# Optimization experiments

Measured on AMD Instinct MI355X. Metric: run time of the kernel, lower is better.

## Reference

```python
import jax, jax.numpy as jnp
import numpy as np
import math

B, M, DM = 4, 4096, 1024
H, HD = 16, 64            # head_dim = hidden_dim // num_heads
SEG, DIL = 128, 2         # segment_size, dilation_rate
BLOCK_M = 64              # kernel query-block size (min(64, M))
SCALE = HD ** -0.5


def _hilbert_map(seq_len):
    # Faithful port of create_hilbert_mapping_fixed (boustrophedon scan).
    if seq_len <= 64:
        return np.arange(seq_len, dtype=np.int32)
    g = int(math.ceil(math.sqrt(seq_len)))
    mp = np.zeros(seq_len, dtype=np.int64)
    idx = 0
    for row in range(g):
        cols = range(g) if row % 2 == 0 else range(g - 1, -1, -1)
        for col in cols:
            if idx < seq_len:
                lp = row * g + col
                if lp < seq_len:
                    mp[lp] = idx
                    idx += 1
    for i in range(seq_len):
        if i >= idx:
            mp[i] = i
    return mp.astype(np.int32)


def setup_inputs() -> dict:
    key = jax.random.key(0)
    k1, k2, k3 = jax.random.split(key, 3)
    x = jax.random.normal(k1, (B, M, DM), jnp.float32)
    Wqkv = jax.random.normal(k2, (3 * DM, DM), jnp.float32) * 0.02
    Wout = jax.random.normal(k3, (DM, DM), jnp.float32) * 0.02
    hmap = jnp.asarray(_hilbert_map(M))
    return {"x": x, "Wqkv": Wqkv, "Wout": Wout, "hmap": hmap}


def _hilbert_attention(x, Wqkv, Wout, hmap):
    Bn, Mn, _ = x.shape
    qkv = x @ Wqkv.T                                   # [B,M,3*DM]
    qkv = qkv.reshape(Bn, Mn, 3, H, HD).transpose(2, 0, 3, 1, 4)
    q, k, v = qkv[0], qkv[1], qkv[2]                   # [B,H,M,HD]

    S = Mn // SEG           # number of segments
    T = SEG // DIL          # keys per segment (dilated offsets 0, DIL, 2*DIL, ...)
    NB = SEG // BLOCK_M     # query blocks per segment

    # Queries gathered through Hilbert map, pre-scaled (as in kernel).
    qh = q[:, :, hmap, :] * SCALE                      # [B,H,M,HD]

    # Dilated key positions per segment, gathered through Hilbert map.
    key_pos = (jnp.arange(S)[:, None] * SEG + jnp.arange(T)[None, :] * DIL).reshape(-1)
    kh = k[:, :, hmap[key_pos], :].reshape(Bn, H, S, T, HD)
    vh = v[:, :, hmap[key_pos], :].reshape(Bn, H, S, T, HD)

    # Scores per (query-block within segment, key): [B,H,S,NB,BLOCK_M,T]
    qs = qh.reshape(Bn, H, S, NB, BLOCK_M, HD)
    scores = jnp.einsum('bhsnqd,bhstd->bhsnqt', qs, kh)

    # Kernel quirk (faithful): per-KEY max taken over the 64-query block,
    # exp accumulated without rescaling -> NOT a true softmax.
    c = jnp.max(scores, axis=4, keepdims=True)         # max over query block
    w = jnp.exp(scores - c)
    num = jnp.einsum('bhsnqt,bhstd->bhsnqd', w, vh)
    den = 1e-10 + jnp.sum(w, axis=-1, keepdims=True)
    out = (num / den).reshape(Bn, H, Mn, HD)

    # Stored at linear (non-Hilbert) positions, then merged heads + out proj.
    out = out.transpose(0, 2, 1, 3).reshape(Bn, Mn, H * HD)
    return out @ Wout.T


def reference(x, Wqkv, Wout, hmap):
    return _hilbert_attention(x, Wqkv, Wout, hmap)
```

## Files before the change

kernel.cpp:

```cpp
#include <hip/hip_runtime.h>
#include <hip/hip_bf16.h>

#define BB 4
#define MM 4096
#define DM 1024
#define NH 16
#define HDIM 64
#define SEGSZ 128
#define NSEG 32
#define ROWS (BB*MM)
#define QKVC (3*DM)
#define KVROWS (BB*MM/2)
#define KVLD 2048
#define NX4  (ROWS*DM/4)
#define NW14 (QKVC*DM/4)
#define NW24 (DM*DM/4)

typedef __attribute__((ext_vector_type(8))) short bf16x8;
typedef __attribute__((ext_vector_type(4))) float f32x4;

__device__ inline unsigned short f2bf(float f) {
  __hip_bfloat16 h = __float2bfloat16(f);
  return *reinterpret_cast<unsigned short*>(&h);
}

__device__ __forceinline__ void gld16(const ushort* g, ushort* l) {
  __builtin_amdgcn_global_load_lds(
      (const __attribute__((address_space(1))) unsigned int*)g,
      (__attribute__((address_space(3))) unsigned int*)l,
      16, 0, 0);
}

__global__ __launch_bounds__(256) void cvt_all(const float4* __restrict__ x,
                                               const float4* __restrict__ w1,
                                               const float4* __restrict__ w2,
                                               ushort4* __restrict__ xo,
                                               ushort4* __restrict__ w1o,
                                               ushort4* __restrict__ w2o) {
  int i = blockIdx.x * 256 + threadIdx.x;
  const float4* src; ushort4* dst; int off;
  if (i < NX4)              { src = x;  dst = xo;  off = i; }
  else if (i < NX4 + NW14)  { src = w1; dst = w1o; off = i - NX4; }
  else                      { src = w2; dst = w2o; off = i - NX4 - NW14; }
  float4 v = src[off];
  ushort4 o;
  o.x = f2bf(v.x); o.y = f2bf(v.y); o.z = f2bf(v.z); o.w = f2bf(v.w);
  dst[off] = o;
}

#define STAGE_A(T, KH, DB) do {                                              \
    gld16(pA0 + (T) * 64 + (KH) * 32,                                        \
          sAB + ((DB) * 2 + (KH)) * 8192 + wave * 512);                      \
    gld16(pA1 + (T) * 64 + (KH) * 32,                                        \
          sAB + ((DB) * 2 + (KH)) * 8192 + 4096 + wave * 512);               \
  } while (0)
#define STAGE_B(T, KH, DB) do {                                              \
    gld16(pB0 + (T) * 64 + (KH) * 32,                                        \
          sAB + 32768 + ((DB) * 2 + (KH)) * 8192 + wave * 512);              \
    gld16(pB1 + (T) * 64 + (KH) * 32,                                        \
          sAB + 32768 + ((DB) * 2 + (KH)) * 8192 + 4096 + wave * 512);       \
  } while (0)
#define VM6 asm volatile("s_waitcnt vmcnt(6)" ::: "memory")
#define VM8 asm volatile("s_waitcnt vmcnt(8)" ::: "memory")
#define VM0 asm volatile("s_waitcnt vmcnt(0)" ::: "memory")
#define NOPS ((void)0)

#define PH_TAIL(CH)                                                          \
    __builtin_amdgcn_s_barrier();                                            \
    asm volatile("s_waitcnt lgkmcnt(0)" ::: "memory");                       \
    __builtin_amdgcn_sched_barrier(0);                                       \
    __builtin_amdgcn_s_setprio(1);                                           \
    _Pragma("unroll")                                                        \
    for (int mf = 0; mf < 8; ++mf)                                           \
      _Pragma("unroll")                                                      \
      for (int nf = 0; nf < 2; ++nf)                                         \
        acc[mf][(CH) * 2 + nf] = __builtin_amdgcn_mfma_f32_16x16x32_bf16(    \
            af[mf], bfv[nf], acc[mf][(CH) * 2 + nf], 0, 0, 0);               \
    __builtin_amdgcn_s_setprio(0);                                           \
    __builtin_amdgcn_s_barrier();

#define PH_F_B(AB, BB_, STAGE, VMA) do {                                     \
    const ushort* Ab = (AB); const ushort* Bb = (BB_);                       \
    _Pragma("unroll")                                                        \
    for (int mf = 0; mf < 8; ++mf) {                                         \
      int r = wm * 128 + mf * 16 + m16;                                      \
      af[mf] = *(const bf16x8*)(Ab + r * 32 + ((quad ^ ((r >> 1) & 3)) << 3)); \
    }                                                                        \
    _Pragma("unroll")                                                        \
    for (int nf = 0; nf < 2; ++nf) {                                         \
      int r = wn * 64 + nf * 16 + m16;                                       \
      bfv[nf] = *(const bf16x8*)(Bb + r * 32 + ((quad ^ ((r >> 1) & 3)) << 3)); \
    }                                                                        \
    STAGE; VMA;                                                              \
    PH_TAIL(0)                                                               \
  } while (0)

#define PH_L_B(BB_, STAGE, VMA) do {                                         \
    const ushort* Bb = (BB_);                                                \
    _Pragma("unroll")                                                        \
    for (int nf = 0; nf < 2; ++nf) {                                         \
      int r = wn * 64 + 32 + nf * 16 + m16;                                  \
      bfv[nf] = *(const bf16x8*)(Bb + r * 32 + ((quad ^ ((r >> 1) & 3)) << 3)); \
    }                                                                        \
    STAGE; VMA;                                                              \
    PH_TAIL(1)                                                               \
  } while (0)

#define PH_F(TB, KH, STAGE, VMA) \
    PH_F_B(sAB + ((TB) * 2 + (KH)) * 8192, sAB + 32768 + ((TB) * 2 + (KH)) * 8192, STAGE, VMA)
#define PH_L(TB, KH, STAGE, VMA) \
    PH_L_B(sAB + 32768 + ((TB) * 2 + (KH)) * 8192, STAGE, VMA)

#define KLOOP_1024                                                           \
  STAGE_A(0, 0, 0); STAGE_B(0, 0, 0);                                        \
  STAGE_A(0, 1, 0); STAGE_B(0, 1, 0);                                        \
  STAGE_A(1, 0, 1); STAGE_B(1, 0, 1);                                        \
  VM8;                                                                       \
  __builtin_amdgcn_s_barrier();                                              \
  _Pragma("unroll 1")                                                        \
  for (int i = 0; i < 7; ++i) {                                              \
    const int t1 = 2 * i + 1, t2 = 2 * i + 2, t3 = 2 * i + 3;                \
    PH_F(0, 0, STAGE_A(t1, 1, 1), NOPS);                                     \
    PH_L(0, 0, STAGE_B(t1, 1, 1), VM6);                                      \
    PH_F(0, 1, STAGE_A(t2, 0, 0), NOPS);                                     \
    PH_L(0, 1, STAGE_B(t2, 0, 0), VM6);                                      \
    PH_F(1, 0, STAGE_A(t2, 1, 0), NOPS);                                     \
    PH_L(1, 0, STAGE_B(t2, 1, 0), VM6);                                      \
    PH_F(1, 1, STAGE_A(t3, 0, 1), NOPS);                                     \
    PH_L(1, 1, STAGE_B(t3, 0, 1), VM6);                                      \
  }                                                                          \
  PH_F(0, 0, STAGE_A(15, 1, 1), NOPS);                                       \
  PH_L(0, 0, STAGE_B(15, 1, 1), VM0);                                        \
  _Pragma("unroll 1")                                                        \
  for (int u = 1; u < 4; ++u) {                                              \
    const ushort* AbU = sAB + u * 8192;                                      \
    const ushort* BbU = sAB + 32768 + u * 8192;                              \
    PH_F_B(AbU, BbU, NOPS, NOPS);                                            \
    PH_L_B(BbU, NOPS, NOPS);                                                 \
  }

__global__ __launch_bounds__(512) void gemm_qkv(const ushort* __restrict__ xbf,
                                                const ushort* __restrict__ wqkv,
                                                ushort* __restrict__ qhb,
                                                ushort* __restrict__ kvb,
                                                const int* __restrict__ hmap,
                                                const int base) {
  __shared__ __align__(16) ushort sAB[65536];
  __shared__ int sRow[256];

  const int blk = blockIdx.x + base;
  const int tid = threadIdx.x;
  const int lane = tid & 63;
  const int wave = tid >> 6;
  const int m16 = lane & 15;
  const int quad = lane >> 4;
  const int wm = wave >> 2;
  const int wn = wave & 3;

  const int j0 = blockIdx.x;
  const int swz = (j0 & 7) * 32 + (j0 >> 3);

  const ushort* Bmat; ushort* C; int row0, col0, N;
  if (blk < 256) {
    row0 = (swz >> 2) * 256; col0 = (swz & 3) * 256;
    Bmat = wqkv; C = qhb; N = DM;
  } else {
    row0 = (swz >> 3) * 256; col0 = (swz & 7) * 256;
    Bmat = wqkv + (size_t)DM * DM; C = kvb; N = KVLD;
  }

  if (tid < 256) {
    int m = row0 + tid, xrow;
    if (blk < 256) {
      int b = m >> 12, p = m & 4095;
      xrow = (b << 12) + hmap[p];
    } else {
      int b = m >> 11, idx = m & 2047;
      int ss = idx >> 6, tt = idx & 63;
      xrow = (b << 12) + hmap[ss * SEGSZ + 2 * tt];
    }
    sRow[tid] = xrow;
  }
  __syncthreads();

  const int f0 = wave * 64 + lane, f1 = 512 + f0;
  const int r0 = f0 >> 2, c0 = (f0 & 3) ^ ((f0 >> 3) & 3);
  const int r1 = f1 >> 2, c1 = (f1 & 3) ^ ((f1 >> 3) & 3);
  const ushort* pA0 = xbf + (size_t)sRow[r0] * DM + c0 * 8;
  const ushort* pA1 = xbf + (size_t)sRow[r1] * DM + c1 * 8;
  const ushort* pB0 = Bmat + (size_t)(col0 + r0) * DM + c0 * 8;
  const ushort* pB1 = Bmat + (size_t)(col0 + r1) * DM + c1 * 8;

  f32x4 acc[8][4] = {};
  bf16x8 af[8], bfv[2];

  KLOOP_1024

#pragma unroll
  for (int mf = 0; mf < 8; ++mf)
#pragma unroll
    for (int rr = 0; rr < 4; ++rr) {
      int row = row0 + wm * 128 + mf * 16 + quad * 4 + rr;
#pragma unroll
      for (int nf = 0; nf < 4; ++nf)
        C[(size_t)row * N + col0 + wn * 64 + nf * 16 + m16] = f2bf(acc[mf][nf][rr]);
    }
}

__global__ __launch_bounds__(512) void gemm_out(const ushort* __restrict__ A,
                                                const ushort* __restrict__ Bmat,
                                                float* __restrict__ C) {
  __shared__ __align__(16) ushort sAB[65536];

  const int tid = threadIdx.x;
  const int lane = tid & 63;
  const int wave = tid >> 6;
  const int m16 = lane & 15;
  const int quad = lane >> 4;
  const int wm = wave >> 2;
  const int wn = wave & 3;

  const int j0 = blockIdx.x;
  const int swz = (j0 & 7) * 32 + (j0 >> 3);
  const int row0 = (swz >> 2) * 256;
  const int col0 = (swz & 3) * 256;

  const int f0 = wave * 64 + lane, f1 = 512 + f0;
  const int r0 = f0 >> 2, c0 = (f0 & 3) ^ ((f0 >> 3) & 3);
  const int r1 = f1 >> 2, c1 = (f1 & 3) ^ ((f1 >> 3) & 3);
  const ushort* pA0 = A + (size_t)(row0 + r0) * DM + c0 * 8;
  const ushort* pA1 = A + (size_t)(row0 + r1) * DM + c1 * 8;
  const ushort* pB0 = Bmat + (size_t)(col0 + r0) * DM + c0 * 8;
  const ushort* pB1 = Bmat + (size_t)(col0 + r1) * DM + c1 * 8;

  f32x4 acc[8][4] = {};
  bf16x8 af[8], bfv[2];

  KLOOP_1024

#pragma unroll
  for (int mf = 0; mf < 8; ++mf)
#pragma unroll
    for (int rr = 0; rr < 4; ++rr) {
      int row = row0 + wm * 128 + mf * 16 + quad * 4 + rr;
#pragma unroll
      for (int nf = 0; nf < 4; ++nf)
        C[(size_t)row * DM + col0 + wn * 64 + nf * 16 + m16] = acc[mf][nf][rr];
    }
}

#undef KLOOP_1024
#undef PH_F
#undef PH_L
#undef PH_F_B
#undef PH_L_B
#undef PH_TAIL
#undef STAGE_A
#undef STAGE_B
#undef VM6
#undef VM8
#undef VM0
#undef NOPS

__global__ __launch_bounds__(256) void attn_kernel(const ushort* __restrict__ qh,
                                                   const ushort* __restrict__ kv,
                                                   ushort* __restrict__ out) {
  __shared__ __align__(16) ushort sQW[128 * 72];
  __shared__ __align__(16) ushort sK[64 * 72];
  __shared__ __align__(16) ushort sVT[64 * 72];
  __shared__ float sCmaxW[4 * 64];
  __shared__ float sDen[128];

  const int bid = blockIdx.x;
  const int s  = bid & 31;
  const int h  = (bid >> 5) & 15;
  const int b  = bid >> 9;
  const int tid = threadIdx.x;
  const int lane = tid & 63;
  const int wave = tid >> 6;
  const int m16 = lane & 15;
  const int quad = lane >> 4;
  const int qb = wave * 32;
  const int hb = wave >> 1;

  {
    const int qr = tid >> 1;
    const int qc = (tid & 1) * 32;
    const ushort* qrow = qh + (size_t)(b * MM + s * SEGSZ + qr) * DM + h * HDIM + qc;
    *(uint4*)(sQW + qr * 72 + qc)      = ((const uint4*)qrow)[0];
    *(uint4*)(sQW + qr * 72 + qc + 8)  = ((const uint4*)qrow)[1];
    *(uint4*)(sQW + qr * 72 + qc + 16) = ((const uint4*)qrow)[2];
    *(uint4*)(sQW + qr * 72 + qc + 24) = ((const uint4*)qrow)[3];

    const int r = tid >> 2;
    const int c = (tid & 3) * 16;
    const ushort* krow = kv + (size_t)(b * (MM/2) + s * 64 + r) * KVLD + h * HDIM + c;
    const ushort* vrow = krow + DM;
    *(uint4*)(sK + r * 72 + c)     = ((const uint4*)krow)[0];
    *(uint4*)(sK + r * 72 + c + 8) = ((const uint4*)krow)[1];
    ushort vv[16];
    *(uint4*)(vv)     = ((const uint4*)vrow)[0];
    *(uint4*)(vv + 8) = ((const uint4*)vrow)[1];
#pragma unroll
    for (int u = 0; u < 16; ++u) sVT[(c + u) * 72 + r] = vv[u];
  }
  __syncthreads();

  f32x4 sc[2][4];
  {
    bf16x8 aq[2][2], bk[4][2];
#pragma unroll
    for (int ks = 0; ks < 2; ++ks) {
#pragma unroll
      for (int ib = 0; ib < 2; ++ib)
        aq[ib][ks] = *(const bf16x8*)(sQW + (qb + ib * 16 + m16) * 72 + ks * 32 + quad * 8);
#pragma unroll
      for (int j = 0; j < 4; ++j)
        bk[j][ks] = *(const bf16x8*)(sK + (j * 16 + m16) * 72 + ks * 32 + quad * 8);
    }
#pragma unroll
    for (int ib = 0; ib < 2; ++ib)
#pragma unroll
      for (int j = 0; j < 4; ++j) {
        f32x4 a = {};
        a = __builtin_amdgcn_mfma_f32_16x16x32_bf16(aq[ib][0], bk[j][0], a, 0, 0, 0);
        a = __builtin_amdgcn_mfma_f32_16x16x32_bf16(aq[ib][1], bk[j][1], a, 0, 0, 0);
        sc[ib][j] = a * 0.125f;
      }
  }

#pragma unroll
  for (int j = 0; j < 4; ++j) {
    float m = -1e30f;
#pragma unroll
    for (int ib = 0; ib < 2; ++ib)
#pragma unroll
      for (int r = 0; r < 4; ++r) m = fmaxf(m, sc[ib][j][r]);
    m = fmaxf(m, __shfl_xor(m, 16));
    m = fmaxf(m, __shfl_xor(m, 32));
    if (quad == 0) sCmaxW[wave * 64 + j * 16 + m16] = m;
  }
  __syncthreads();

  {
    float part[2][4] = {};
#pragma unroll
    for (int j = 0; j < 4; ++j) {
      const int col = j * 16 + m16;
      float c0 = fmaxf(sCmaxW[hb * 128 + col], sCmaxW[hb * 128 + 64 + col]);
#pragma unroll
      for (int ib = 0; ib < 2; ++ib)
#pragma unroll
        for (int r = 0; r < 4; ++r) {
          float ww = __expf(sc[ib][j][r] - c0);
          sc[ib][j][r] = ww;
          part[ib][r] += ww;
        }
    }
#pragma unroll
    for (int ib = 0; ib < 2; ++ib)
#pragma unroll
      for (int r = 0; r < 4; ++r) {
        float p = part[ib][r];
        p += __shfl_xor(p, 1); p += __shfl_xor(p, 2);
        p += __shfl_xor(p, 4); p += __shfl_xor(p, 8);
        if (m16 == 0) sDen[qb + ib * 16 + quad * 4 + r] = p;
      }
#pragma unroll
    for (int ib = 0; ib < 2; ++ib)
#pragma unroll
      for (int j = 0; j < 4; ++j)
#pragma unroll
        for (int r = 0; r < 4; ++r)
          sQW[(qb + ib * 16 + quad * 4 + r) * 72 + j * 16 + m16] = f2bf(sc[ib][j][r]);
  }
  __syncthreads();

  f32x4 o[2][4] = {};
  {
    bf16x8 aw[2][2], bv[4][2];
#pragma unroll
    for (int ks = 0; ks < 2; ++ks) {
#pragma unroll
      for (int ib = 0; ib < 2; ++ib)
        aw[ib][ks] = *(const bf16x8*)(sQW + (qb + ib * 16 + m16) * 72 + ks * 32 + quad * 8);
#pragma unroll
      for (int j = 0; j < 4; ++j)
        bv[j][ks] = *(const bf16x8*)(sVT + (j * 16 + m16) * 72 + ks * 32 + quad * 8);
    }
#pragma unroll
    for (int ib = 0; ib < 2; ++ib)
#pragma unroll
      for (int j = 0; j < 4; ++j) {
        o[ib][j] = __builtin_amdgcn_mfma_f32_16x16x32_bf16(aw[ib][0], bv[j][0], o[ib][j], 0, 0, 0);
        o[ib][j] = __builtin_amdgcn_mfma_f32_16x16x32_bf16(aw[ib][1], bv[j][1], o[ib][j], 0, 0, 0);
      }
  }

#pragma unroll
  for (int ib = 0; ib < 2; ++ib)
#pragma unroll
    for (int r = 0; r < 4; ++r) {
      const int lrow = qb + ib * 16 + quad * 4 + r;
      float rd = 1.0f / (1e-10f + sDen[lrow]);
      ushort* op = out + (size_t)(b * MM + s * SEGSZ + lrow) * DM + h * HDIM + m16;
#pragma unroll
      for (int j = 0; j < 4; ++j)
        op[j * 16] = f2bf(o[ib][j][r] * rd);
    }
}

extern "C" void kernel_launch(void* const* d_in, const int* in_sizes, int n_in,
                              void* d_out, int out_size, void* d_ws, size_t ws_size,
                              hipStream_t stream) {
  const float* x    = (const float*)d_in[0];
  const float* wqkv = (const float*)d_in[1];
  const float* wout = (const float*)d_in[2];
  const int*   hmap = (const int*)d_in[3];
  float* outp = (float*)d_out;

  ushort* xbf    = (ushort*)d_ws;
  ushort* wqkvbf = xbf + (size_t)ROWS * DM;
  ushort* woutbf = wqkvbf + (size_t)QKVC * DM;
  ushort* qhb    = woutbf + (size_t)DM * DM;
  ushort* kvb    = qhb + (size_t)ROWS * DM;
  ushort* attn   = kvb + (size_t)KVROWS * KVLD;

  cvt_all<<<(NX4 + NW14 + NW24 + 255) / 256, 256, 0, stream>>>(
      (const float4*)x, (const float4*)wqkv, (const float4*)wout,
      (ushort4*)xbf, (ushort4*)wqkvbf, (ushort4*)woutbf);

  gemm_qkv<<<256, 512, 0, stream>>>(xbf, wqkvbf, qhb, kvb, hmap, 0);
  gemm_qkv<<<256, 512, 0, stream>>>(xbf, wqkvbf, qhb, kvb, hmap, 256);

  attn_kernel<<<BB * NH * NSEG, 256, 0, stream>>>(qhb, kvb, attn);

  gemm_out<<<256, 512, 0, stream>>>(attn, woutbf, outp);
}
```

Measured before the change: 262.4 us.

## Halve GEMM LDS buffering and merge QKV GEMM launches into one grid

Shrinks the GEMM shared-memory staging from a deep double-buffered 128KB ring to a 64KB single-tile scheme that prefetches the next half-tile while computing the current one. The smaller LDS footprint is meant to let two 512-thread blocks share a CU, and the two QKV GEMM launches become one 512-block grid. Together these aim to raise occupancy and remove a launch boundary. The cost is a shallower prefetch, with less latency hiding per block.

```diff
diff --git a/kernel.cpp b/kernel.cpp
--- a/kernel.cpp
+++ b/kernel.cpp
@@ -48,20 +48,15 @@
   dst[off] = o;
 }
 
-#define STAGE_A(T, KH, DB) do {                                              \
-    gld16(pA0 + (T) * 64 + (KH) * 32,                                        \
-          sAB + ((DB) * 2 + (KH)) * 8192 + wave * 512);                      \
-    gld16(pA1 + (T) * 64 + (KH) * 32,                                        \
-          sAB + ((DB) * 2 + (KH)) * 8192 + 4096 + wave * 512);               \
+#define STAGE_A(T, KH) do {                                                  \
+    gld16(pA0 + (T) * 64 + (KH) * 32, sAB + (KH) * 8192 + wave * 512);       \
+    gld16(pA1 + (T) * 64 + (KH) * 32, sAB + (KH) * 8192 + 4096 + wave * 512);\
   } while (0)
-#define STAGE_B(T, KH, DB) do {                                              \
-    gld16(pB0 + (T) * 64 + (KH) * 32,                                        \
-          sAB + 32768 + ((DB) * 2 + (KH)) * 8192 + wave * 512);              \
-    gld16(pB1 + (T) * 64 + (KH) * 32,                                        \
-          sAB + 32768 + ((DB) * 2 + (KH)) * 8192 + 4096 + wave * 512);       \
+#define STAGE_B(T, KH) do {                                                  \
+    gld16(pB0 + (T) * 64 + (KH) * 32, sAB + 16384 + (KH) * 8192 + wave * 512);\
+    gld16(pB1 + (T) * 64 + (KH) * 32, sAB + 16384 + (KH) * 8192 + 4096 + wave * 512);\
   } while (0)
-#define VM6 asm volatile("s_waitcnt vmcnt(6)" ::: "memory")
-#define VM8 asm volatile("s_waitcnt vmcnt(8)" ::: "memory")
+#define VM2 asm volatile("s_waitcnt vmcnt(2)" ::: "memory")
 #define VM0 asm volatile("s_waitcnt vmcnt(0)" ::: "memory")
 #define NOPS ((void)0)
 
@@ -106,49 +101,30 @@
     PH_TAIL(1)                                                               \
   } while (0)
 
-#define PH_F(TB, KH, STAGE, VMA) \
-    PH_F_B(sAB + ((TB) * 2 + (KH)) * 8192, sAB + 32768 + ((TB) * 2 + (KH)) * 8192, STAGE, VMA)
-#define PH_L(TB, KH, STAGE, VMA) \
-    PH_L_B(sAB + 32768 + ((TB) * 2 + (KH)) * 8192, STAGE, VMA)
-
 #define KLOOP_1024                                                           \
-  STAGE_A(0, 0, 0); STAGE_B(0, 0, 0);                                        \
-  STAGE_A(0, 1, 0); STAGE_B(0, 1, 0);                                        \
-  STAGE_A(1, 0, 1); STAGE_B(1, 0, 1);                                        \
-  VM8;                                                                       \
+  STAGE_A(0, 0); STAGE_B(0, 0); STAGE_A(0, 1);                               \
+  VM2;                                                                       \
   __builtin_amdgcn_s_barrier();                                              \
   _Pragma("unroll 1")                                                        \
-  for (int i = 0; i < 7; ++i) {                                              \
-    const int t1 = 2 * i + 1, t2 = 2 * i + 2, t3 = 2 * i + 3;                \
-    PH_F(0, 0, STAGE_A(t1, 1, 1), NOPS);                                     \
-    PH_L(0, 0, STAGE_B(t1, 1, 1), VM6);                                      \
-    PH_F(0, 1, STAGE_A(t2, 0, 0), NOPS);                                     \
-    PH_L(0, 1, STAGE_B(t2, 0, 0), VM6);                                      \
-    PH_F(1, 0, STAGE_A(t2, 1, 0), NOPS);                                     \
-    PH_L(1, 0, STAGE_B(t2, 1, 0), VM6);                                      \
-    PH_F(1, 1, STAGE_A(t3, 0, 1), NOPS);                                     \
-    PH_L(1, 1, STAGE_B(t3, 0, 1), VM6);                                      \
-  }                                                                          \
-  PH_F(0, 0, STAGE_A(15, 1, 1), NOPS);                                       \
-  PH_L(0, 0, STAGE_B(15, 1, 1), VM0);                                        \
-  _Pragma("unroll 1")                                                        \
-  for (int u = 1; u < 4; ++u) {                                              \
-    const ushort* AbU = sAB + u * 8192;                                      \
-    const ushort* BbU = sAB + 32768 + u * 8192;                              \
-    PH_F_B(AbU, BbU, NOPS, NOPS);                                            \
-    PH_L_B(BbU, NOPS, NOPS);                                                 \
+  for (int t = 0; t < 16; ++t) {                                             \
+    PH_F_B(sAB, sAB + 16384, STAGE_B(t, 1), NOPS);                           \
+    if (t < 15) { PH_L_B(sAB + 16384, STAGE_A(t + 1, 0), VM2); }             \
+    else        { PH_L_B(sAB + 16384, NOPS, VM0); }                          \
+    if (t < 15) { PH_F_B(sAB + 8192, sAB + 24576, STAGE_B(t + 1, 0), NOPS); }\
+    else        { PH_F_B(sAB + 8192, sAB + 24576, NOPS, NOPS); }             \
+    if (t < 15) { PH_L_B(sAB + 24576, STAGE_A(t + 1, 1), VM2); }             \
+    else        { PH_L_B(sAB + 24576, NOPS, NOPS); }                         \
   }
 
 __global__ __launch_bounds__(512) void gemm_qkv(const ushort* __restrict__ xbf,
                                                 const ushort* __restrict__ wqkv,
                                                 ushort* __restrict__ qhb,
                                                 ushort* __restrict__ kvb,
-                                                const int* __restrict__ hmap,
-                                                const int base) {
-  __shared__ __align__(16) ushort sAB[65536];
+                                                const int* __restrict__ hmap) {
+  __shared__ __align__(16) ushort sAB[32768];
   __shared__ int sRow[256];
 
-  const int blk = blockIdx.x + base;
+  const int blk = blockIdx.x;
   const int tid = threadIdx.x;
   const int lane = tid & 63;
   const int wave = tid >> 6;
@@ -157,7 +133,7 @@
   const int wm = wave >> 2;
   const int wn = wave & 3;
 
-  const int j0 = blockIdx.x;
+  const int j0 = blk & 255;
   const int swz = (j0 & 7) * 32 + (j0 >> 3);
 
   const ushort* Bmat; ushort* C; int row0, col0, N;
@@ -210,7 +186,7 @@
 __global__ __launch_bounds__(512) void gemm_out(const ushort* __restrict__ A,
                                                 const ushort* __restrict__ Bmat,
                                                 float* __restrict__ C) {
-  __shared__ __align__(16) ushort sAB[65536];
+  __shared__ __align__(16) ushort sAB[32768];
 
   const int tid = threadIdx.x;
   const int lane = tid & 63;
@@ -250,15 +226,12 @@
 }
 
 #undef KLOOP_1024
-#undef PH_F
-#undef PH_L
 #undef PH_F_B
 #undef PH_L_B
 #undef PH_TAIL
 #undef STAGE_A
 #undef STAGE_B
-#undef VM6
-#undef VM8
+#undef VM2
 #undef VM0
 #undef NOPS
 
@@ -430,8 +403,7 @@
       (const float4*)x, (const float4*)wqkv, (const float4*)wout,
       (ushort4*)xbf, (ushort4*)wqkvbf, (ushort4*)woutbf);
 
-  gemm_qkv<<<256, 512, 0, stream>>>(xbf, wqkvbf, qhb, kvb, hmap, 0);
-  gemm_qkv<<<256, 512, 0, stream>>>(xbf, wqkvbf, qhb, kvb, hmap, 256);
+  gemm_qkv<<<512, 512, 0, stream>>>(xbf, wqkvbf, qhb, kvb, hmap);
 
   attn_kernel<<<BB * NH * NSEG, 256, 0, stream>>>(qhb, kvb, attn);
 
```

After: 565.9 us. 116% more time.
